# Kernel optimization log

Measured on AMD Instinct MI355X. Metric: run time of the kernel, lower is better.

Reference implementation:

```python
import jax, jax.numpy as jnp
import numpy as np

BOUND = 1.0
N_RAYS = 2048
TOT = 128        # num_steps (samples per pixel)
IND_S = 16       # indicator_steps
MAX_DEPTHS = 2
HID = 64
EPS = 1e-8


def setup_inputs() -> dict:
    key = jax.random.key(0)
    ks = jax.random.split(key, 13)
    M = N_RAYS * TOT
    rays_o = 0.3 * jax.random.normal(ks[0], (N_RAYS, 3), jnp.float32)
    rd = jax.random.normal(ks[1], (N_RAYS, 3), jnp.float32)
    rays_d = rd / (jnp.linalg.norm(rd, axis=-1, keepdims=True) + EPS)
    env_map = 0.1 * jax.random.normal(ks[2], (3, 128, 256), jnp.float32)
    Wd1 = jax.random.normal(ks[3], (3, HID), jnp.float32) / np.sqrt(3.0)
    Wd2 = jax.random.normal(ks[4], (HID, 3), jnp.float32) / np.sqrt(HID)
    Wf1 = jax.random.normal(ks[5], (6, HID), jnp.float32) / np.sqrt(6.0)
    Ws = jax.random.normal(ks[6], (HID, 3), jnp.float32) / np.sqrt(HID)
    Wdir = jax.random.normal(ks[7], (HID, 3), jnp.float32) / np.sqrt(HID)
    Wrho = jax.random.normal(ks[8], (HID, 3), jnp.float32) / np.sqrt(HID)
    jitter = jax.random.uniform(ks[9], (MAX_DEPTHS, M, IND_S), jnp.float32)
    u_t = jax.random.uniform(ks[10], (MAX_DEPTHS, M), jnp.float32)
    u_scatter = jax.random.uniform(ks[11], (MAX_DEPTHS, M), jnp.float32)
    channel = jax.random.randint(ks[12], (MAX_DEPTHS, M), 0, 3)
    return dict(rays_o=rays_o, rays_d=rays_d, env_map=env_map, Wd1=Wd1, Wd2=Wd2,
                Wf1=Wf1, Ws=Ws, Wdir=Wdir, Wrho=Wrho,
                jitter=jitter, u_t=u_t, u_scatter=u_scatter, channel=channel)


def _density(pts, Wd1, Wd2):
    # stand-in NeRF density field: 3 spectral channels, positive
    return jax.nn.softplus(jnp.sin(pts @ Wd1) @ Wd2)


def _material(o, d, Wf1, Ws, Wdir, Wrho):
    f = jnp.tanh(jnp.concatenate([o, d], axis=-1) @ Wf1)
    sigma_t = jax.nn.softplus(f @ Ws)                     # [M,3]
    dn = f @ Wdir
    d_out = dn / (jnp.linalg.norm(dn, axis=-1, keepdims=True) + EPS)
    fused_rho = jax.nn.sigmoid(f @ Wrho)                  # [M,3]
    return sigma_t, d_out, fused_rho


def _sample_env(env_map, p):
    # equirectangular lookup == torch grid_sample(bilinear, align_corners=False, zero pad)
    x, y, z = p[:, 0], p[:, 1], p[:, 2]
    theta = jnp.nan_to_num(jnp.arctan2(x, -z)) / jnp.pi            # grid x in [-1,1]
    phi = 2.0 / jnp.pi * jnp.nan_to_num(jnp.arccos(y)) - 1.0       # grid y in [-1,1]
    C, H, W = env_map.shape
    ix = ((theta + 1.0) * W - 1.0) * 0.5
    iy = ((phi + 1.0) * H - 1.0) * 0.5
    x0 = jnp.floor(ix); y0 = jnp.floor(iy)
    wx = ix - x0; wy = iy - y0

    def tap(xc, yc, w):
        inb = (xc >= 0) & (xc < W) & (yc >= 0) & (yc < H)
        xi = jnp.clip(xc, 0, W - 1).astype(jnp.int32)
        yi = jnp.clip(yc, 0, H - 1).astype(jnp.int32)
        return (w * inb)[:, None] * env_map[:, yi, xi].T   # [M,3]

    v = (tap(x0, y0, (1 - wx) * (1 - wy)) + tap(x0 + 1, y0, wx * (1 - wy)) +
         tap(x0, y0 + 1, (1 - wx) * wy) + tap(x0 + 1, y0 + 1, wx * wy))
    return jnp.exp(v)


def _render(rays_o, rays_d, env_map, Wd1, Wd2, Wf1, Ws, Wdir, Wrho,
            jitter, u_t, u_scatter, channel):
    M = N_RAYS * TOT
    o = jnp.repeat(rays_o, TOT, axis=0)   # [M,3]
    d = jnp.repeat(rays_d, TOT, axis=0)
    alive = jnp.ones((M,), bool)          # masked version of boolean compaction
    thr = jnp.ones((M, 3), jnp.float32)
    rgbs = jnp.zeros((M, 3), jnp.float32)
    lin = jnp.linspace(0.0, 1.0, IND_S)

    for dep in range(MAX_DEPTHS):
        # ray-sphere intersection (radius=bound)
        a = jnp.sum(d * d, -1)
        b = 2.0 * jnp.sum(d * o, -1)
        c = jnp.sum(o * o, -1) - BOUND ** 2
        delta = b * b - 4.0 * a * c
        alive = alive & (delta > 0.0)
        sq = jnp.sqrt(jnp.maximum(delta, 0.0))
        nears = jnp.maximum((-b - sq) / (2.0 * a), 0.001)
        fars = jnp.maximum((-b + sq) / (2.0 * a), 0.001)
        span = fars - nears

        # stratified indicator samples -> per-channel majorant
        z = nears[:, None] + span[:, None] * lin[None, :]
        z = z + (jitter[dep] - 0.5) * (span[:, None] / IND_S)
        pts = o[:, None, :] + d[:, None, :] * z[:, :, None]          # [M,S,3]
        sigma = _density(pts.reshape(-1, 3), Wd1, Wd2).reshape(M, IND_S, 3)
        ch = channel[dep]
        maj_multi = jnp.maximum(sigma.max(axis=1), 0.001)            # [M,3]
        sig_ch = jnp.take_along_axis(sigma, ch[:, None, None], axis=2)[..., 0]
        maj = jnp.maximum(sig_ch.max(axis=1), 0.001)                 # [M]

        # free-flight sampling (last depth forces hit at far boundary)
        if dep < MAX_DEPTHS - 1:
            t = -jnp.log1p(-u_t[dep]) / maj + nears
        else:
            t = fars
        hit = alive & (t >= fars)

        # environment hit contribution
        denom = jnp.exp(-maj_multi * span[:, None]) / (maj_multi.max(-1, keepdims=True) + EPS) + EPS
        Le = _sample_env(env_map, o + d * fars[:, None])
        contrib = thr * (denom / jax.lax.stop_gradient(denom.mean(-1, keepdims=True))) * Le
        rgbs = rgbs + jnp.where(hit[:, None], contrib, 0.0)
        alive = alive & ~hit
        if dep == MAX_DEPTHS - 1:
            break

        # throughput update + null/real scattering (delta tracking)
        trans = jnp.exp(-maj_multi * (t - nears)[:, None]) / maj_multi.max(-1, keepdims=True)
        den2 = jax.lax.stop_gradient((maj_multi * trans).mean(-1, keepdims=True))
        thr = jnp.where(alive[:, None], thr * trans / den2, thr)
        o = jnp.where(alive[:, None], jax.lax.stop_gradient(o + d * t[:, None]), o)
        sigma_t, d_out, fused_rho = _material(o, d, Wf1, Ws, Wdir, Wrho)
        sp = jnp.minimum(jnp.take_along_axis(sigma_t, ch[:, None], axis=1)[:, 0] / maj, 1.0)
        sm = alive & (u_scatter[dep] < sp)
        d = jnp.where(sm[:, None], d_out, d)
        thr = jnp.where(sm[:, None], thr / (sp[:, None] + EPS) * fused_rho,
              jnp.where(alive[:, None], thr / (1.0 - sp[:, None] + EPS), thr))

    return rgbs.reshape(N_RAYS, TOT, 3).mean(axis=1)   # [N,3]


def reference(rays_o, rays_d, env_map, Wd1, Wd2, Wf1, Ws, Wdir, Wrho,
              jitter, u_t, u_scatter, channel):
    return _render(rays_o, rays_d, env_map, Wd1, Wd2, Wf1, Ws, Wdir, Wrho,
                   jitter, u_t, u_scatter, channel)
```

## Files before the change

kernel.cpp:

```cpp
#include <hip/hip_runtime.h>
#include <math.h>

#define NRAYS 2048
#define TOT   128
#define INDS  16
#define HID   64
#define EPSF  1e-8f
#define MTOT  (NRAYS*TOT)
#define NTAB  128

typedef float f32x2 __attribute__((ext_vector_type(2)));
typedef float f32x4 __attribute__((ext_vector_type(4)));

__device__ __forceinline__ float rcp_f(float x) {
    return __builtin_amdgcn_rcpf(x);
}
__device__ __forceinline__ float softplus_f(float x) {
    return fmaxf(x, 0.0f) + __logf(1.0f + __expf(-fabsf(x)));
}
__device__ __forceinline__ float sigmoid_f(float x) {
    return rcp_f(1.0f + __expf(-x));
}
__device__ __forceinline__ float tanh_fast(float x) {
    float e2 = __expf(2.0f * x);
    return 1.0f - 2.0f * rcp_f(e2 + 1.0f);
}
__device__ __forceinline__ f32x2 pkmax(f32x2 a, f32x2 b) {
    f32x2 r; r.x = fmaxf(a.x, b.x); r.y = fmaxf(a.y, b.y); return r;
}
__device__ __forceinline__ f32x2 pkfma(f32x2 a, f32x2 b, f32x2 c) {
    return __builtin_elementwise_fma(a, b, c);
}

#define CK(i) ((float)(i)*(1.0f/15.0f) - 0.03125f)

#define MAKE_Z(jA, jB, kbase, nears, span)                                    \
    float s16 = (span) * (1.0f/16.0f);                                        \
    f32x2 z01, z23, z45, z67;                                                 \
    z01.x = fmaf((jA).x, s16, fmaf(span, CK((kbase)+0), nears));              \
    z01.y = fmaf((jA).y, s16, fmaf(span, CK((kbase)+1), nears));              \
    z23.x = fmaf((jA).z, s16, fmaf(span, CK((kbase)+2), nears));              \
    z23.y = fmaf((jA).w, s16, fmaf(span, CK((kbase)+3), nears));              \
    z45.x = fmaf((jB).x, s16, fmaf(span, CK((kbase)+4), nears));              \
    z45.y = fmaf((jB).y, s16, fmaf(span, CK((kbase)+5), nears));              \
    z67.x = fmaf((jB).z, s16, fmaf(span, CK((kbase)+6), nears));              \
    z67.y = fmaf((jB).w, s16, fmaf(span, CK((kbase)+7), nears));

#define TAB_EVAL(zz, mx0, mx1, mx2)                                           \
    {                                                                         \
        float x = ((zz) - ztab0) * invh;                                      \
        x = fminf(fmaxf(x, 0.0f), (float)(NTAB-1) - 1e-3f);                   \
        int i = (int)x; float w = x - (float)i;                               \
        float ta0 = sT0[i], tb0 = sT0[i+1];                                   \
        float ta1 = sT1[i], tb1 = sT1[i+1];                                   \
        float ta2 = sT2[i], tb2 = sT2[i+1];                                   \
        mx0 = fmaxf(mx0, fmaf(w, tb0 - ta0, ta0));                            \
        mx1 = fmaxf(mx1, fmaf(w, tb1 - ta1, ta1));                            \
        mx2 = fmaxf(mx2, fmaf(w, tb2 - ta2, ta2));                            \
    }

__device__ __forceinline__ void env_logv(
    const float* __restrict__ env_map,
    float px, float py, float pz,
    float& v0, float& v1, float& v2)
{
    float theta = atan2f(px, -pz) * (1.0f/3.14159265358979323846f);
    float acv = (fabsf(py) <= 1.0f) ? acosf(py) : 0.0f;
    float phi = 0.63661977236758134308f * acv - 1.0f;
    float ixf = ((theta + 1.0f)*256.0f - 1.0f)*0.5f;
    float iyf = ((phi   + 1.0f)*128.0f - 1.0f)*0.5f;
    float x0f = floorf(ixf), y0f = floorf(iyf);
    float wx = ixf - x0f, wy = iyf - y0f;
    v0 = 0.f; v1 = 0.f; v2 = 0.f;
    auto tap = [&](float xc, float yc, float w) {
        if (xc >= 0.0f && xc < 256.0f && yc >= 0.0f && yc < 128.0f) {
            int xi = (int)xc, yi = (int)yc;
            const float* e = env_map + yi*256 + xi;
            v0 += w * e[0];
            v1 += w * e[128*256];
            v2 += w * e[2*128*256];
        }
    };
    tap(x0f,      y0f,      (1.0f-wx)*(1.0f-wy));
    tap(x0f+1.0f, y0f,      wx*(1.0f-wy));
    tap(x0f,      y0f+1.0f, (1.0f-wx)*wy);
    tap(x0f+1.0f, y0f+1.0f, wx*wy);
}

__global__ __launch_bounds__(256)
void render_kernel(const float* __restrict__ rays_o,
                   const float* __restrict__ rays_d,
                   const float* __restrict__ env_map,
                   const float* __restrict__ Wd1,
                   const float* __restrict__ Wd2,
                   const float* __restrict__ Wf1,
                   const float* __restrict__ Ws,
                   const float* __restrict__ Wdir,
                   const float* __restrict__ Wrho,
                   const float* __restrict__ jitter,
                   const float* __restrict__ u_t,
                   const float* __restrict__ u_scatter,
                   const int*   __restrict__ channel,
                   float* __restrict__ out)
{
    const int ray  = blockIdx.x;
    const int tid  = threadIdx.x;
    const int s    = tid >> 1;
    const int half = tid & 1;
    const int m    = ray * TOT + s;
    const int kbase = half * 8;

    __shared__ f32x4 sAB[HID];
    __shared__ f32x4 sW01[HID];
    __shared__ f32x2 sW2[HID];
    __shared__ f32x4 sPW[HID];
    __shared__ f32x4 sM0[HID];
    __shared__ f32x4 sM1[HID];
    __shared__ f32x4 sM2[HID];
    __shared__ float sT0[NTAB];
    __shared__ float sT1[NTAB];
    __shared__ float sT2[NTAB];
    __shared__ f32x4 sP0[TOT];
    __shared__ f32x4 sP1[TOT];
    __shared__ f32x2 sP2[TOT];
    __shared__ float sEnvE[3];
    __shared__ int   sCnt;
    __shared__ float sred[4][3];

    const float4* j0p = (const float4*)(jitter + (size_t)m*INDS + kbase);
    float4 j0A = j0p[0], j0B = j0p[1];
    const float4* j1p = (const float4*)(jitter + ((size_t)MTOT + m)*INDS + kbase);
    float4 j1A = j1p[0], j1B = j1p[1];
    int   ch = channel[m];
    float ut = u_t[m];
    float us = u_scatter[m];

    float ox = rays_o[ray*3+0], oy = rays_o[ray*3+1], oz = rays_o[ray*3+2];
    float dx = rays_d[ray*3+0], dy = rays_d[ray*3+1], dz = rays_d[ray*3+2];

    if (tid == 0) sCnt = 0;
    if (tid < HID) {
        const float INV2PI = 0.15915494309189535f;
        float w1x = Wd1[tid], w1y = Wd1[HID+tid], w1z = Wd1[2*HID+tid];
        float pw1x = w1x*INV2PI, pw1y = w1y*INV2PI, pw1z = w1z*INV2PI;
        float A = ox*pw1x + oy*pw1y + oz*pw1z;
        float B = dx*pw1x + dy*pw1y + dz*pw1z;
        float w20 = Wd2[3*tid], w21 = Wd2[3*tid+1], w22 = Wd2[3*tid+2];
        sAB[tid]  = (f32x4){A, A, B, B};
        sW01[tid] = (f32x4){w20, w20, w21, w21};
        sW2[tid]  = (f32x2){w22, w22};
        sPW[tid]  = (f32x4){pw1x, pw1y, pw1z, 0.0f};
        float f0 = Wf1[tid],       f1 = Wf1[HID+tid],   f2 = Wf1[2*HID+tid];
        float f3 = Wf1[3*HID+tid], f4 = Wf1[4*HID+tid], f5 = Wf1[5*HID+tid];
        float P = ox*f0 + oy*f1 + oz*f2 + dx*f3 + dy*f4 + dz*f5;
        float Q = dx*f0 + dy*f1 + dz*f2;
        sM0[tid] = (f32x4){P, Q, Ws[3*tid], Ws[3*tid+1]};
        sM1[tid] = (f32x4){Ws[3*tid+2], Wdir[3*tid], Wdir[3*tid+1], Wdir[3*tid+2]};
        sM2[tid] = (f32x4){Wrho[3*tid], Wrho[3*tid+1], Wrho[3*tid+2], 0.0f};
    }
    __syncthreads();

    float a0g = dx*dx + dy*dy + dz*dz;
    float b0g = 2.0f*(dx*ox + dy*oy + dz*oz);
    float c0g = (ox*ox + oy*oy + oz*oz) - 1.0f;
    float delta0 = b0g*b0g - 4.0f*a0g*c0g;
    bool alive = (delta0 > 0.0f);

    float nears = 0.f, fars = 0.f, span = 0.f, ztab0 = 0.f, invh = 0.f;
    if (alive) {
        float sq = sqrtf(delta0);
        float inv2a = rcp_f(a0g + a0g);
        nears = fmaxf((-b0g - sq) * inv2a, 0.001f);
        fars  = fmaxf((-b0g + sq) * inv2a, 0.001f);
        span  = fars - nears;
        ztab0 = fmaf(-span, 0.03125f, nears);
        float width = span * 1.0625f;
        float hstep = width * (1.0f/(NTAB-1));
        invh = (float)(NTAB-1) * rcp_f(width);
        int p = tid >> 1;
        float zp = fmaf((float)p, hstep, ztab0);
        float f0 = 0.f, f1 = 0.f, f2 = 0.f;
        const int jb = half * 32;
        #pragma unroll 4
        for (int j = jb; j < jb + 32; ++j) {
            f32x4 ab  = sAB[j];
            f32x4 w01 = sW01[j];
            f32x2 w2  = sW2[j];
            float hv = __builtin_amdgcn_sinf(fmaf(zp, ab.z, ab.x));
            f0 = fmaf(hv, w01.x, f0);
            f1 = fmaf(hv, w01.z, f1);
            f2 = fmaf(hv, w2.x, f2);
        }
        f0 += __shfl_xor(f0, 1, 64);
        f1 += __shfl_xor(f1, 1, 64);
        f2 += __shfl_xor(f2, 1, 64);
        if (half == 0) { sT0[p] = f0; sT1[p] = f1; sT2[p] = f2; }
        if (tid == 0) {
            float v0,v1,v2;
            env_logv(env_map, fmaf(dx,fars,ox), fmaf(dy,fars,oy), fmaf(dz,fars,oz),
                     v0,v1,v2);
            sEnvE[0] = __expf(v0); sEnvE[1] = __expf(v1); sEnvE[2] = __expf(v2);
        }
    }
    __syncthreads();

    float thr0 = 1.f, thr1 = 1.f, thr2 = 1.f;
    float rgb0 = 0.f, rgb1 = 0.f, rgb2 = 0.f;
    bool  tab_d1 = false;
    float tadv = 0.f;

    if (alive) {
        MAKE_Z(j0A, j0B, kbase, nears, span)
        float mx0 = -1e30f, mx1 = -1e30f, mx2 = -1e30f;
        TAB_EVAL(z01.x, mx0,mx1,mx2) TAB_EVAL(z01.y, mx0,mx1,mx2)
        TAB_EVAL(z23.x, mx0,mx1,mx2) TAB_EVAL(z23.y, mx0,mx1,mx2)
        TAB_EVAL(z45.x, mx0,mx1,mx2) TAB_EVAL(z45.y, mx0,mx1,mx2)
        TAB_EVAL(z67.x, mx0,mx1,mx2) TAB_EVAL(z67.y, mx0,mx1,mx2)
        mx0 = fmaxf(mx0, __shfl_xor(mx0, 1, 64));
        mx1 = fmaxf(mx1, __shfl_xor(mx1, 1, 64));
        mx2 = fmaxf(mx2, __shfl_xor(mx2, 1, 64));

        float maj0 = fmaxf(softplus_f(mx0), 0.001f);
        float maj1 = fmaxf(softplus_f(mx1), 0.001f);
        float maj2 = fmaxf(softplus_f(mx2), 0.001f);
        float mmax = fmaxf(fmaxf(maj0, maj1), maj2);

        float maj = (ch == 0) ? maj0 : ((ch == 1) ? maj1 : maj2);
        float t   = fmaf(-__logf(1.0f - ut), rcp_f(maj), nears);

        if (t >= fars) {
            float im   = rcp_f(mmax + EPSF);
            float den0 = fmaf(__expf(-maj0*span), im, EPSF);
            float den1 = fmaf(__expf(-maj1*span), im, EPSF);
            float den2 = fmaf(__expf(-maj2*span), im, EPSF);
            float idm = 3.0f * rcp_f(den0+den1+den2);
            rgb0 = den0*idm*sEnvE[0];
            rgb1 = den1*idm*sEnvE[1];
            rgb2 = den2*idm*sEnvE[2];
        } else {
            float tn  = t - nears;
            float imm = rcp_f(mmax);
            float tr0 = __expf(-maj0*tn) * imm;
            float tr1 = __expf(-maj1*tn) * imm;
            float tr2 = __expf(-maj2*tn) * imm;
            float i2m = 3.0f * rcp_f(maj0*tr0 + maj1*tr1 + maj2*tr2);
            thr0 = tr0 * i2m;
            thr1 = tr1 * i2m;
            thr2 = tr2 * i2m;
            ox = fmaf(dx, t, ox); oy = fmaf(dy, t, oy); oz = fmaf(dz, t, oz);

            float st0=0.f, st1=0.f, st2=0.f;
            float dn0=0.f, dn1=0.f, dn2v=0.f;
            float rh0=0.f, rh1=0.f, rh2=0.f;
            const int j0 = half * 32;
            #pragma unroll 2
            for (int j = j0; j < j0 + 32; ++j) {
                f32x4 q0 = sM0[j];
                f32x4 q1 = sM1[j];
                f32x4 q2 = sM2[j];
                float pre = fmaf(t, q0.y, q0.x);
                float f = tanh_fast(pre);
                st0  = fmaf(f, q0.z, st0);
                st1  = fmaf(f, q0.w, st1);
                st2  = fmaf(f, q1.x, st2);
                dn0  = fmaf(f, q1.y, dn0);
                dn1  = fmaf(f, q1.z, dn1);
                dn2v = fmaf(f, q1.w, dn2v);
                rh0  = fmaf(f, q2.x, rh0);
                rh1  = fmaf(f, q2.y, rh1);
                rh2  = fmaf(f, q2.z, rh2);
            }
            st0  += __shfl_xor(st0, 1, 64);
            st1  += __shfl_xor(st1, 1, 64);
            st2  += __shfl_xor(st2, 1, 64);
            dn0  += __shfl_xor(dn0, 1, 64);
            dn1  += __shfl_xor(dn1, 1, 64);
            dn2v += __shfl_xor(dn2v, 1, 64);
            rh0  += __shfl_xor(rh0, 1, 64);
            rh1  += __shfl_xor(rh1, 1, 64);
            rh2  += __shfl_xor(rh2, 1, 64);

            float stch = (ch == 0) ? st0 : ((ch == 1) ? st1 : st2);
            float sp = fminf(softplus_f(stch) * rcp_f(maj), 1.0f);
            if (us < sp) {
                float inr = rcp_f(sqrtf(dn0*dn0 + dn1*dn1 + dn2v*dn2v) + EPSF);
                float ndx = dn0*inr, ndy = dn1*inr, ndz = dn2v*inr;
                float isp = rcp_f(sp + EPSF);
                float t0 = thr0 * isp * sigmoid_f(rh0);
                float t1 = thr1 * isp * sigmoid_f(rh1);
                float t2 = thr2 * isp * sigmoid_f(rh2);
                if (half == 0) {
                    int sl = atomicAdd(&sCnt, 1);
                    sP0[sl] = (f32x4){ox, oy, oz, ndx};
                    sP1[sl] = (f32x4){ndy, ndz, t0, t1};
                    sP2[sl] = (f32x2){t2, (float)m};
                }
            } else {
                float iv = rcp_f(1.0f - sp + EPSF);
                thr0 *= iv; thr1 *= iv; thr2 *= iv;
                tab_d1 = true;
                tadv = t;
            }
        }
    }
    __syncthreads();
    int npool = sCnt;

    if (tab_d1) {
        float fars1 = fmaxf(fars - tadv, 0.001f);
        float span1 = fars1 - 0.001f;
        float n1    = tadv + 0.001f;
        MAKE_Z(j1A, j1B, kbase, n1, span1)
        float mx0 = -1e30f, mx1 = -1e30f, mx2 = -1e30f;
        TAB_EVAL(z01.x, mx0,mx1,mx2) TAB_EVAL(z01.y, mx0,mx1,mx2)
        TAB_EVAL(z23.x, mx0,mx1,mx2) TAB_EVAL(z23.y, mx0,mx1,mx2)
        TAB_EVAL(z45.x, mx0,mx1,mx2) TAB_EVAL(z45.y, mx0,mx1,mx2)
        TAB_EVAL(z67.x, mx0,mx1,mx2) TAB_EVAL(z67.y, mx0,mx1,mx2)
        mx0 = fmaxf(mx0, __shfl_xor(mx0, 1, 64));
        mx1 = fmaxf(mx1, __shfl_xor(mx1, 1, 64));
        mx2 = fmaxf(mx2, __shfl_xor(mx2, 1, 64));

        float maj0 = fmaxf(softplus_f(mx0), 0.001f);
        float maj1 = fmaxf(softplus_f(mx1), 0.001f);
        float maj2 = fmaxf(softplus_f(mx2), 0.001f);
        float mmax = fmaxf(fmaxf(maj0, maj1), maj2);

        float im   = rcp_f(mmax + EPSF);
        float den0 = fmaf(__expf(-maj0*span1), im, EPSF);
        float den1 = fmaf(__expf(-maj1*span1), im, EPSF);
        float den2 = fmaf(__expf(-maj2*span1), im, EPSF);
        float idm = 3.0f * rcp_f(den0+den1+den2);
        rgb0 += thr0 * den0*idm*sEnvE[0];
        rgb1 += thr1 * den1*idm*sEnvE[1];
        rgb2 += thr2 * den2*idm*sEnvE[2];
    }

    {
        const int qlane = tid & 3;
        const int kq    = qlane * 4;
        const float kqf = (float)kq;
        for (int q = tid >> 2; q < npool; q += 64) {
            f32x4 p0 = sP0[q];
            f32x4 p1 = sP1[q];
            f32x2 p2 = sP2[q];
            float pox = p0.x, poy = p0.y, poz = p0.z;
            float pdx = p0.w, pdy = p1.x, pdz = p1.y;
            float pt0 = p1.z, pt1 = p1.w, pt2 = p2.x;
            int   mm  = (int)p2.y;

            float a1 = pdx*pdx + pdy*pdy + pdz*pdz;
            float b1 = 2.0f*(pdx*pox + pdy*poy + pdz*poz);
            float c1 = (pox*pox + poy*poy + poz*poz) - 1.0f;
            float delta1 = b1*b1 - 4.0f*a1*c1;
            if (delta1 > 0.0f) {
                const float4* jp = (const float4*)(jitter + ((size_t)MTOT + mm)*INDS + kq);
                float4 jq = jp[0];
                float sq1    = sqrtf(delta1);
                float inv2a1 = rcp_f(a1 + a1);
                float nears1 = fmaxf((-b1 - sq1) * inv2a1, 0.001f);
                float fars1  = fmaxf((-b1 + sq1) * inv2a1, 0.001f);
                float span1  = fars1 - nears1;
                float s16q   = span1 * (1.0f/16.0f);
                f32x2 zA, zB;
                zA.x = fmaf(jq.x, s16q, fmaf(span1, (kqf+0.0f)*(1.0f/15.0f) - 0.03125f, nears1));
                zA.y = fmaf(jq.y, s16q, fmaf(span1, (kqf+1.0f)*(1.0f/15.0f) - 0.03125f, nears1));
                zB.x = fmaf(jq.z, s16q, fmaf(span1, (kqf+2.0f)*(1.0f/15.0f) - 0.03125f, nears1));
                zB.y = fmaf(jq.w, s16q, fmaf(span1, (kqf+3.0f)*(1.0f/15.0f) - 0.03125f, nears1));

                f32x2 a0A = {0.f,0.f}, a0B = {0.f,0.f};
                f32x2 a1A = {0.f,0.f}, a1B = {0.f,0.f};
                f32x2 a2A = {0.f,0.f}, a2B = {0.f,0.f};
                #pragma unroll 2
                for (int j = 0; j < HID; ++j) {
                    f32x4 pw  = sPW[j];
                    f32x4 w01 = sW01[j];
                    f32x2 w2  = sW2[j];
                    float A = fmaf(pox, pw.x, fmaf(poy, pw.y, poz*pw.z));
                    float B = fmaf(pdx, pw.x, fmaf(pdy, pw.y, pdz*pw.z));
                    f32x2 A2 = {A, A}, B2 = {B, B};
                    f32x2 gA = pkfma(zA, B2, A2);
                    f32x2 gB = pkfma(zB, B2, A2);
                    f32x2 hA, hB;
                    hA.x = __builtin_amdgcn_sinf(gA.x); hA.y = __builtin_amdgcn_sinf(gA.y);
                    hB.x = __builtin_amdgcn_sinf(gB.x); hB.y = __builtin_amdgcn_sinf(gB.y);
                    f32x2 W0 = {w01.x, w01.y}, W1 = {w01.z, w01.w};
                    a0A = pkfma(hA, W0, a0A); a0B = pkfma(hB, W0, a0B);
                    a1A = pkfma(hA, W1, a1A); a1B = pkfma(hB, W1, a1B);
                    a2A = pkfma(hA, w2, a2A); a2B = pkfma(hB, w2, a2B);
                }
                f32x2 pm0 = pkmax(a0A, a0B);
                f32x2 pm1 = pkmax(a1A, a1B);
                f32x2 pm2 = pkmax(a2A, a2B);
                float mx0 = fmaxf(pm0.x, pm0.y);
                float mx1 = fmaxf(pm1.x, pm1.y);
                float mx2 = fmaxf(pm2.x, pm2.y);
                mx0 = fmaxf(mx0, __shfl_xor(mx0, 1, 64));
                mx1 = fmaxf(mx1, __shfl_xor(mx1, 1, 64));
                mx2 = fmaxf(mx2, __shfl_xor(mx2, 1, 64));
                mx0 = fmaxf(mx0, __shfl_xor(mx0, 2, 64));
                mx1 = fmaxf(mx1, __shfl_xor(mx1, 2, 64));
                mx2 = fmaxf(mx2, __shfl_xor(mx2, 2, 64));

                float maj0 = fmaxf(softplus_f(mx0), 0.001f);
                float maj1 = fmaxf(softplus_f(mx1), 0.001f);
                float maj2 = fmaxf(softplus_f(mx2), 0.001f);
                float mmax = fmaxf(fmaxf(maj0, maj1), maj2);

                float im   = rcp_f(mmax + EPSF);
                float den0 = fmaf(__expf(-maj0*span1), im, EPSF);
                float den1 = fmaf(__expf(-maj1*span1), im, EPSF);
                float den2 = fmaf(__expf(-maj2*span1), im, EPSF);
                float idm = 3.0f * rcp_f(den0+den1+den2);
                float v0,v1,v2;
                env_logv(env_map, fmaf(pdx,fars1,pox), fmaf(pdy,fars1,poy),
                         fmaf(pdz,fars1,poz), v0,v1,v2);
                if (qlane < 2) {
                    rgb0 += pt0 * den0*idm*__expf(v0);
                    rgb1 += pt1 * den1*idm*__expf(v1);
                    rgb2 += pt2 * den2*idm*__expf(v2);
                }
            }
        }
    }

    float r0 = rgb0, r1 = rgb1, r2 = rgb2;
    #pragma unroll
    for (int off = 32; off > 0; off >>= 1) {
        r0 += __shfl_down(r0, off, 64);
        r1 += __shfl_down(r1, off, 64);
        r2 += __shfl_down(r2, off, 64);
    }
    int wave = tid >> 6;
    if ((tid & 63) == 0) {
        sred[wave][0] = r0; sred[wave][1] = r1; sred[wave][2] = r2;
    }
    __syncthreads();
    if (tid == 0) {
        out[ray*3+0] = (sred[0][0]+sred[1][0]+sred[2][0]+sred[3][0]) * (1.0f/256.0f);
        out[ray*3+1] = (sred[0][1]+sred[1][1]+sred[2][1]+sred[3][1]) * (1.0f/256.0f);
        out[ray*3+2] = (sred[0][2]+sred[1][2]+sred[2][2]+sred[3][2]) * (1.0f/256.0f);
    }
}

extern "C" void kernel_launch(void* const* d_in, const int* in_sizes, int n_in,
                              void* d_out, int out_size, void* d_ws, size_t ws_size,
                              hipStream_t stream) {
    const float* rays_o    = (const float*)d_in[0];
    const float* rays_d    = (const float*)d_in[1];
    const float* env_map   = (const float*)d_in[2];
    const float* Wd1       = (const float*)d_in[3];
    const float* Wd2       = (const float*)d_in[4];
    const float* Wf1       = (const float*)d_in[5];
    const float* Ws        = (const float*)d_in[6];
    const float* Wdir      = (const float*)d_in[7];
    const float* Wrho      = (const float*)d_in[8];
    const float* jitter    = (const float*)d_in[9];
    const float* u_t       = (const float*)d_in[10];
    const float* u_scatter = (const float*)d_in[11];
    const int*   channel   = (const int*)d_in[12];
    float* out = (float*)d_out;

    render_kernel<<<dim3(NRAYS), dim3(256), 0, stream>>>(
        rays_o, rays_d, env_map, Wd1, Wd2, Wf1, Ws, Wdir, Wrho,
        jitter, u_t, u_scatter, channel, out);
}
```

Before: 161.2 us.

## Offload scattered-path pool evaluation to a global load-balanced second kernel

Per-block pools of scattered rays, whose second-bounce work is uneven across rays, are compacted into a global workspace buffer through an atomic counter. A second kernel then processes the whole pool with a grid-stride loop and adds results into the output with atomics. This is meant to remove load imbalance where a few blocks with large pools set the tail latency. It costs an extra launch, a memset, global writes and reads of the pool, float atomics on the output, and the output must already hold the first kernel's value before the atomics accumulate onto it.

```diff
diff --git a/kernel.cpp b/kernel.cpp
--- a/kernel.cpp
+++ b/kernel.cpp
@@ -8,6 +8,7 @@
 #define EPSF  1e-8f
 #define MTOT  (NRAYS*TOT)
 #define NTAB  128
+#define POOL_GRID 2048
 
 typedef float f32x2 __attribute__((ext_vector_type(2)));
 typedef float f32x4 __attribute__((ext_vector_type(4)));
@@ -101,6 +102,11 @@
                    const float* __restrict__ u_t,
                    const float* __restrict__ u_scatter,
                    const int*   __restrict__ channel,
+                   unsigned int* __restrict__ g_count,
+                   float4* __restrict__ e0g,
+                   float4* __restrict__ e1g,
+                   float2* __restrict__ e2g,
+                   int cap,
                    float* __restrict__ out)
 {
     const int ray  = blockIdx.x;
@@ -125,6 +131,7 @@
     __shared__ f32x2 sP2[TOT];
     __shared__ float sEnvE[3];
     __shared__ int   sCnt;
+    __shared__ int   sGbase;
     __shared__ float sred[4][3];
 
     const float4* j0p = (const float4*)(jitter + (size_t)m*INDS + kbase);
@@ -306,6 +313,31 @@
     __syncthreads();
     int npool = sCnt;
 
+    if (tid == 0) {
+        sGbase = (cap > 0 && npool > 0)
+               ? (int)atomicAdd(g_count, (unsigned int)npool) : 0;
+    }
+    __syncthreads();
+    int gbase = sGbase;
+    for (int i = tid; i < npool; i += 256) {
+        int gi = gbase + i;
+        if (gi < cap) {
+            f32x4 a = sP0[i]; f32x4 b = sP1[i]; f32x2 c = sP2[i];
+            e0g[gi] = make_float4(a.x, a.y, a.z, a.w);
+            e1g[gi] = make_float4(b.x, b.y, b.z, b.w);
+            e2g[gi] = make_float2(c.x, c.y);
+        }
+    }
+    int qstart = npool;
+    if (cap > 0) {
+        int fit = cap - gbase;
+        if (fit < 0) fit = 0;
+        if (fit > npool) fit = npool;
+        qstart = fit;
+    } else {
+        qstart = 0;
+    }
+
     if (tab_d1) {
         float fars1 = fmaxf(fars - tadv, 0.001f);
         float span1 = fars1 - 0.001f;
@@ -339,7 +371,7 @@
         const int qlane = tid & 3;
         const int kq    = qlane * 4;
         const float kqf = (float)kq;
-        for (int q = tid >> 2; q < npool; q += 64) {
+        for (int q = qstart + (tid >> 2); q < npool; q += 64) {
             f32x4 p0 = sP0[q];
             f32x4 p1 = sP1[q];
             f32x2 p2 = sP2[q];
@@ -442,6 +474,120 @@
     }
 }
 
+__global__ __launch_bounds__(256)
+void pool_kernel(const float* __restrict__ env_map,
+                 const float* __restrict__ Wd1,
+                 const float* __restrict__ Wd2,
+                 const float* __restrict__ jitter,
+                 const unsigned int* __restrict__ g_count,
+                 const float4* __restrict__ e0g,
+                 const float4* __restrict__ e1g,
+                 const float2* __restrict__ e2g,
+                 int cap,
+                 float* __restrict__ out)
+{
+    __shared__ f32x4 sPW4[HID];
+    __shared__ f32x2 sW22[HID];
+    const int tid = threadIdx.x;
+    if (tid < HID) {
+        const float INV2PI = 0.15915494309189535f;
+        sPW4[tid] = (f32x4){Wd1[tid]*INV2PI, Wd1[HID+tid]*INV2PI,
+                            Wd1[2*HID+tid]*INV2PI, Wd2[3*tid]};
+        sW22[tid] = (f32x2){Wd2[3*tid+1], Wd2[3*tid+2]};
+    }
+    __syncthreads();
+
+    int count = (int)*g_count;
+    if (count > cap) count = cap;
+
+    const int qlane = tid & 3;
+    const int kq    = qlane * 4;
+    const float kqf = (float)kq;
+
+    for (int idx = blockIdx.x*64 + (tid >> 2); idx < count; idx += gridDim.x*64) {
+        float4 p0 = e0g[idx];
+        float4 p1 = e1g[idx];
+        float2 p2 = e2g[idx];
+        float pox = p0.x, poy = p0.y, poz = p0.z;
+        float pdx = p0.w, pdy = p1.x, pdz = p1.y;
+        float pt0 = p1.z, pt1 = p1.w, pt2 = p2.x;
+        int   mm  = (int)p2.y;
+
+        float a1 = pdx*pdx + pdy*pdy + pdz*pdz;
+        float b1 = 2.0f*(pdx*pox + pdy*poy + pdz*poz);
+        float c1 = (pox*pox + poy*poy + poz*poz) - 1.0f;
+        float delta1 = b1*b1 - 4.0f*a1*c1;
+        if (delta1 > 0.0f) {
+            const float4* jp = (const float4*)(jitter + ((size_t)MTOT + mm)*INDS + kq);
+            float4 jq = jp[0];
+            float sq1    = sqrtf(delta1);
+            float inv2a1 = rcp_f(a1 + a1);
+            float nears1 = fmaxf((-b1 - sq1) * inv2a1, 0.001f);
+            float fars1  = fmaxf((-b1 + sq1) * inv2a1, 0.001f);
+            float span1  = fars1 - nears1;
+            float s16q   = span1 * (1.0f/16.0f);
+            f32x2 zA, zB;
+            zA.x = fmaf(jq.x, s16q, fmaf(span1, (kqf+0.0f)*(1.0f/15.0f) - 0.03125f, nears1));
+            zA.y = fmaf(jq.y, s16q, fmaf(span1, (kqf+1.0f)*(1.0f/15.0f) - 0.03125f, nears1));
+            zB.x = fmaf(jq.z, s16q, fmaf(span1, (kqf+2.0f)*(1.0f/15.0f) - 0.03125f, nears1));
+            zB.y = fmaf(jq.w, s16q, fmaf(span1, (kqf+3.0f)*(1.0f/15.0f) - 0.03125f, nears1));
+
+            f32x2 a0A = {0.f,0.f}, a0B = {0.f,0.f};
+            f32x2 a1A = {0.f,0.f}, a1B = {0.f,0.f};
+            f32x2 a2A = {0.f,0.f}, a2B = {0.f,0.f};
+            #pragma unroll 2
+            for (int j = 0; j < HID; ++j) {
+                f32x4 pw  = sPW4[j];
+                f32x2 w22 = sW22[j];
+                float A = fmaf(pox, pw.x, fmaf(poy, pw.y, poz*pw.z));
+                float B = fmaf(pdx, pw.x, fmaf(pdy, pw.y, pdz*pw.z));
+                f32x2 A2 = {A, A}, B2 = {B, B};
+                f32x2 gA = pkfma(zA, B2, A2);
+                f32x2 gB = pkfma(zB, B2, A2);
+                f32x2 hA, hB;
+                hA.x = __builtin_amdgcn_sinf(gA.x); hA.y = __builtin_amdgcn_sinf(gA.y);
+                hB.x = __builtin_amdgcn_sinf(gB.x); hB.y = __builtin_amdgcn_sinf(gB.y);
+                f32x2 W0 = {pw.w, pw.w}, W1 = {w22.x, w22.x}, W2v = {w22.y, w22.y};
+                a0A = pkfma(hA, W0, a0A); a0B = pkfma(hB, W0, a0B);
+                a1A = pkfma(hA, W1, a1A); a1B = pkfma(hB, W1, a1B);
+                a2A = pkfma(hA, W2v, a2A); a2B = pkfma(hB, W2v, a2B);
+            }
+            f32x2 pm0 = pkmax(a0A, a0B);
+            f32x2 pm1 = pkmax(a1A, a1B);
+            f32x2 pm2 = pkmax(a2A, a2B);
+            float mx0 = fmaxf(pm0.x, pm0.y);
+            float mx1 = fmaxf(pm1.x, pm1.y);
+            float mx2 = fmaxf(pm2.x, pm2.y);
+            mx0 = fmaxf(mx0, __shfl_xor(mx0, 1, 64));
+            mx1 = fmaxf(mx1, __shfl_xor(mx1, 1, 64));
+            mx2 = fmaxf(mx2, __shfl_xor(mx2, 1, 64));
+            mx0 = fmaxf(mx0, __shfl_xor(mx0, 2, 64));
+            mx1 = fmaxf(mx1, __shfl_xor(mx1, 2, 64));
+            mx2 = fmaxf(mx2, __shfl_xor(mx2, 2, 64));
+
+            float maj0 = fmaxf(softplus_f(mx0), 0.001f);
+            float maj1 = fmaxf(softplus_f(mx1), 0.001f);
+            float maj2 = fmaxf(softplus_f(mx2), 0.001f);
+            float mmax = fmaxf(fmaxf(maj0, maj1), maj2);
+
+            float im   = rcp_f(mmax + EPSF);
+            float den0 = fmaf(__expf(-maj0*span1), im, EPSF);
+            float den1 = fmaf(__expf(-maj1*span1), im, EPSF);
+            float den2 = fmaf(__expf(-maj2*span1), im, EPSF);
+            float idm = 3.0f * rcp_f(den0+den1+den2);
+            float v0,v1,v2;
+            env_logv(env_map, fmaf(pdx,fars1,pox), fmaf(pdy,fars1,poy),
+                     fmaf(pdz,fars1,poz), v0,v1,v2);
+            if (qlane == 0) {
+                int ray = mm >> 7;
+                atomicAdd(&out[ray*3+0], pt0*den0*idm*__expf(v0)*(1.0f/128.0f));
+                atomicAdd(&out[ray*3+1], pt1*den1*idm*__expf(v1)*(1.0f/128.0f));
+                atomicAdd(&out[ray*3+2], pt2*den2*idm*__expf(v2)*(1.0f/128.0f));
+            }
+        }
+    }
+}
+
 extern "C" void kernel_launch(void* const* d_in, const int* in_sizes, int n_in,
                               void* d_out, int out_size, void* d_ws, size_t ws_size,
                               hipStream_t stream) {
@@ -460,7 +606,31 @@
     const int*   channel   = (const int*)d_in[12];
     float* out = (float*)d_out;
 
+    int cap = 0;
+    unsigned int* g_count = nullptr;
+    float4* e0g = nullptr; float4* e1g = nullptr; float2* e2g = nullptr;
+    if (d_ws && ws_size >= 4096) {
+        long c = ((long)ws_size - 256) / 40;
+        if (c > MTOT) c = MTOT;
+        cap = (int)c;
+        char* base = (char*)d_ws;
+        g_count = (unsigned int*)base;
+        e0g = (float4*)(base + 256);
+        e1g = (float4*)(base + 256 + (size_t)cap*16);
+        e2g = (float2*)(base + 256 + (size_t)cap*32);
+    }
+
+    if (cap > 0) {
+        hipMemsetAsync(d_ws, 0, 4, stream);
+    }
+
     render_kernel<<<dim3(NRAYS), dim3(256), 0, stream>>>(
         rays_o, rays_d, env_map, Wd1, Wd2, Wf1, Ws, Wdir, Wrho,
-        jitter, u_t, u_scatter, channel, out);
-}
+        jitter, u_t, u_scatter, channel,
+        g_count, e0g, e1g, e2g, cap, out);
+
+    if (cap > 0) {
+        pool_kernel<<<dim3(POOL_GRID), dim3(256), 0, stream>>>(
+            env_map, Wd1, Wd2, jitter, g_count, e0g, e1g, e2g, cap, out);
+    }
+}
```

Result: slower. 206.0 us (+27.8%).
